# Performance work log

Hardware: AMD Instinct MI355X
Metric: run time of the kernel (lower is better)

Reference implementation:

```python
import jax, jax.numpy as jnp
import numpy as np

N_NODES = 50000
N_EDGES = 800000
IN_C = 64
OUT_C = 64
HEADS = 4
N_LAYERS = 2
BN_EPS = 1e-5
NEG_SLOPE = 0.2


def setup_inputs() -> dict:
    key = jax.random.key(0)
    ks = jax.random.split(key, 20)
    inp = {
        "x": jax.random.normal(ks[0], (N_NODES, IN_C), dtype=jnp.float32),
        "edge_index": jax.random.randint(ks[1], (2, N_EDGES), 0, N_NODES, dtype=jnp.int64),
        "edge_weight": jax.random.uniform(ks[2], (N_EDGES,), dtype=jnp.float32),
    }
    # per-layer GATConv + BN params (glorot-ish init)
    for i in range(N_LAYERS):
        k = 3 + i * 5
        scale = 1.0 / np.sqrt(IN_C)
        inp[f"W{i}"] = jax.random.normal(ks[k], (IN_C, HEADS * OUT_C), dtype=jnp.float32) * scale
        inp[f"asrc{i}"] = jax.random.normal(ks[k + 1], (HEADS, OUT_C), dtype=jnp.float32) * scale
        inp[f"adst{i}"] = jax.random.normal(ks[k + 2], (HEADS, OUT_C), dtype=jnp.float32) * scale
        inp[f"b{i}"] = jnp.zeros((OUT_C,), dtype=jnp.float32)
        inp[f"gamma{i}"] = jnp.ones((OUT_C,), dtype=jnp.float32)
        inp[f"beta{i}"] = jnp.zeros((OUT_C,), dtype=jnp.float32)
    return inp


def _gat_layer(x, src, dst, W, a_src, a_dst, b):
    # x: [N, C_in]; src/dst: [E'] (with self loops). Per-head dim = OUT_C.
    xh = (x @ W).reshape(-1, HEADS, OUT_C)          # [N, H, C]
    al_src = jnp.sum(xh * a_src[None], axis=-1)      # [N, H]
    al_dst = jnp.sum(xh * a_dst[None], axis=-1)      # [N, H]
    e = jax.nn.leaky_relu(al_src[src] + al_dst[dst], NEG_SLOPE)  # [E', H]
    # segment softmax over edges sharing a destination node
    m = jax.lax.stop_gradient(jax.ops.segment_max(e, dst, num_segments=N_NODES))
    p = jnp.exp(e - m[dst])
    denom = jax.ops.segment_sum(p, dst, num_segments=N_NODES)
    alpha = p / (denom[dst] + 1e-16)                 # [E', H]
    out = jax.ops.segment_sum(alpha[:, :, None] * xh[src], dst, num_segments=N_NODES)  # [N,H,C]
    return out.mean(axis=1) + b                      # concat=False -> mean over heads


def _batchnorm(x, gamma, beta):
    mu = x.mean(axis=0)
    var = x.var(axis=0)
    return gamma * (x - mu) * jax.lax.rsqrt(var + BN_EPS) + beta


def reference(x, edge_index, edge_weight, W0, asrc0, adst0, b0, gamma0, beta0,
              W1, asrc1, adst1, b1, gamma1, beta1):
    # edge_weight is passed as edge_attr to PyG GATConv but edge_dim=None -> ignored.
    loop = jnp.arange(N_NODES, dtype=edge_index.dtype)
    src = jnp.concatenate([edge_index[0], loop])  # add_self_loops=True (PyG default)
    dst = jnp.concatenate([edge_index[1], loop])
    params = [(W0, asrc0, adst0, b0, gamma0, beta0),
              (W1, asrc1, adst1, b1, gamma1, beta1)]
    saved = None
    for (W, a_s, a_d, b, g, bt) in params:
        x = _gat_layer(x, src, dst, W, a_s, a_d, b)
        saved = x
        x = _batchnorm(x, g, bt)
        x = jax.nn.relu(x)
        # dropout(0.5) is identity in eval mode
    return (x, saved)
```

## Files before the change

kernel.cpp:

```cpp
#include <hip/hip_runtime.h>
#include <stdint.h>

#define NEG_SLOPE 0.2f
#define BN_EPS 1e-5f

typedef __attribute__((ext_vector_type(8))) short bf16x8;
typedef __attribute__((ext_vector_type(4))) float f32x4;

__device__ __forceinline__ float bf2f(unsigned short u) {
  union { unsigned int i; float f; } v; v.i = ((unsigned int)u) << 16; return v.f;
}
__device__ __forceinline__ float asf(unsigned int u) {
  union { unsigned int i; float f; } v; v.i = u; return v.f;
}
__device__ __forceinline__ unsigned short f2bf(float f) {
  union { float f; unsigned int i; } v; v.f = f;
  unsigned int i = v.i;
  return (unsigned short)((i + 0x7fffu + ((i >> 16) & 1u)) >> 16);
}
__device__ __forceinline__ float loadF(const void* p, long long i, int f32) {
  return f32 ? ((const float*)p)[i] : bf2f(((const unsigned short*)p)[i]);
}
__device__ __forceinline__ int edge_at(const void* ei, long long idx, int is64) {
  return is64 ? (int)((const long long*)ei)[idx] : ((const int*)ei)[idx];
}

__global__ void detect_kernel(const unsigned short* __restrict__ x,
                              const int* __restrict__ ei32,
                              int* __restrict__ flags) {
  __shared__ int wild, oddnz;
  if (threadIdx.x == 0) { wild = 0; oddnz = 0; }
  __syncthreads();
  int lw = 0, lo = 0;
  for (int i = threadIdx.x; i < 4096; i += 256) {
    unsigned short u = x[i];
    int ex = (u >> 7) & 0xFF;
    if (ex >= 0x86) lw++;
    if (ei32[2 * i + 1] != 0) lo++;
  }
  if (lw) atomicAdd(&wild, lw);
  if (lo) atomicAdd(&oddnz, lo);
  __syncthreads();
  if (threadIdx.x == 0) { flags[0] = (wild > 64) ? 1 : 0; flags[1] = (oddnz == 0) ? 1 : 0; }
}

__global__ __launch_bounds__(256) void wtrans_kernel(
    const void* __restrict__ W0, const void* __restrict__ as0, const void* __restrict__ ad0,
    const void* __restrict__ W1, const void* __restrict__ as1, const void* __restrict__ ad1,
    const int* __restrict__ flags, int layer1_bf16,
    unsigned short* __restrict__ WTx0, unsigned short* __restrict__ WTx1) {
  const void* W = blockIdx.x ? W1 : W0;
  const void* asrc = blockIdx.x ? as1 : as0;
  const void* adst = blockIdx.x ? ad1 : ad0;
  unsigned short* WTx = blockIdx.x ? WTx1 : WTx0;
  int f32 = flags[0];
  __shared__ unsigned short Wl[64 * 258];
  int t = threadIdx.x;
  for (int i = t; i < 64 * 256; i += 256) {
    int k = i >> 8, c = i & 255;
    Wl[k * 258 + c] = f32 ? f2bf(((const float*)W)[i]) : ((const unsigned short*)W)[i];
  }
  __syncthreads();
  {
    int c = t;
    #pragma unroll
    for (int k8 = 0; k8 < 64; k8 += 8) {
      unsigned int p0 = (unsigned int)Wl[(k8 + 0) * 258 + c] | ((unsigned int)Wl[(k8 + 1) * 258 + c] << 16);
      unsigned int p1 = (unsigned int)Wl[(k8 + 2) * 258 + c] | ((unsigned int)Wl[(k8 + 3) * 258 + c] << 16);
      unsigned int p2 = (unsigned int)Wl[(k8 + 4) * 258 + c] | ((unsigned int)Wl[(k8 + 5) * 258 + c] << 16);
      unsigned int p3 = (unsigned int)Wl[(k8 + 6) * 258 + c] | ((unsigned int)Wl[(k8 + 7) * 258 + c] << 16);
      uint4 pk; pk.x = p0; pk.y = p1; pk.z = p2; pk.w = p3;
      *(uint4*)&WTx[c * 64 + k8] = pk;
    }
  }
  for (int idx = t; idx < 512; idx += 256) {
    int r = idx >> 6;
    int k = idx & 63;
    int h = r & 3;
    const void* av = (r >> 2) ? adst : asrc;
    float acc = 0.f;
    #pragma unroll 8
    for (int c = 0; c < 64; c++)
      acc += bf2f(Wl[k * 258 + h * 64 + c]) * loadF(av, h * 64 + c, f32);
    WTx[(256 + r) * 64 + k] = f2bf(acc);
  }
  for (int idx = t; idx < 512; idx += 256) WTx[264 * 64 + idx] = 0;
}

__global__ __launch_bounds__(256) void hist_kernel(const void* __restrict__ ei, int E, int N,
                                                   const int* __restrict__ flags,
                                                   int* __restrict__ deg) {
  int e = blockIdx.x * 256 + threadIdx.x;
  if (e >= E) return;
  int is64 = flags[1];
  int d = edge_at(ei, (long long)E + e, is64);
  d = (d < 0 || d >= N) ? 0 : d;
  atomicAdd(&deg[d], 1);
}

__global__ __launch_bounds__(256) void partial_kernel(const int* __restrict__ deg,
                                                      int* __restrict__ blocksum, int N) {
  int t = threadIdx.x;
  int idx = blockIdx.x * 256 + t;
  int v = (idx < N) ? deg[idx] : 0;
  #pragma unroll
  for (int o = 1; o < 64; o <<= 1) v += __shfl_xor(v, o);
  __shared__ int ws[4];
  if ((t & 63) == 0) ws[t >> 6] = v;
  __syncthreads();
  if (t == 0) blocksum[blockIdx.x] = ws[0] + ws[1] + ws[2] + ws[3];
}

__global__ void scan_base_kernel(const int* __restrict__ blocksum,
                                 int* __restrict__ blockbase, int B) {
  int lane = threadIdx.x;
  int base = 0;
  if (lane == 0) blockbase[0] = 0;
  for (int start = 0; start < B; start += 64) {
    int idx = start + lane;
    int v = (idx < B) ? blocksum[idx] : 0;
    int sc = v;
    #pragma unroll
    for (int o = 1; o < 64; o <<= 1) {
      int u = __shfl_up(sc, o);
      if (lane >= o) sc += u;
    }
    if (idx < B) blockbase[idx + 1] = base + sc;
    base = __shfl(base + sc, 63);
  }
}

__global__ __launch_bounds__(256) void scan_final_kernel(const int* __restrict__ deg,
                                                         const int* __restrict__ blockbase,
                                                         int* __restrict__ offsets, int N) {
  int t = threadIdx.x;
  int lane = t & 63;
  int wid = t >> 6;
  int idx = blockIdx.x * 256 + t;
  int v = (idx < N) ? deg[idx] : 0;
  int sc = v;
  #pragma unroll
  for (int o = 1; o < 64; o <<= 1) {
    int u = __shfl_up(sc, o);
    if (lane >= o) sc += u;
  }
  __shared__ int ws[4];
  if (lane == 63) ws[wid] = sc;
  __syncthreads();
  int add = 0;
  #pragma unroll
  for (int w = 0; w < 4; w++) if (w < wid) add += ws[w];
  if (idx < N) offsets[idx + 1] = blockbase[blockIdx.x] + add + sc;
  if (idx == 0) offsets[0] = 0;
}

__global__ __launch_bounds__(256) void scatter_kernel(
    const void* __restrict__ ei, int E, int N, const int* __restrict__ flags,
    const int* __restrict__ offsets, int* __restrict__ cursor,
    int* __restrict__ csr_src) {
  int e = blockIdx.x * 256 + threadIdx.x;
  if (e >= E) return;
  int is64 = flags[1];
  int s = edge_at(ei, e, is64);
  int d = edge_at(ei, (long long)E + e, is64);
  s = (s < 0 || s >= N) ? 0 : s;
  d = (d < 0 || d >= N) ? 0 : d;
  int pos = offsets[d] + atomicAdd(&cursor[d], 1);
  csr_src[pos] = s;
}

__global__ __launch_bounds__(256, 2) void gemm_mfma(
    const void* __restrict__ x, const unsigned short* __restrict__ WTx,
    const int* __restrict__ flags, int x_flex,
    unsigned short* __restrict__ xh, float* __restrict__ als, float* __restrict__ ald,
    int N) {
  __shared__ unsigned short RP[4][16 * 264];
  int f32 = flags[0];
  int xf = x_flex ? f32 : 0;
  int t = threadIdx.x;
  int wave = t >> 6, lane = t & 63;
  int q = lane >> 4, r16 = lane & 15;
  int m0 = blockIdx.x * 64 + wave * 16;
  if (m0 >= N) return;
  int row = m0 + r16;
  int rowc = row < N ? row : N - 1;

  bf16x8 a0, a1;
  if (xf) {
    const float* xp = (const float*)x + (size_t)rowc * 64 + q * 8;
    float4 v0 = ((const float4*)xp)[0];
    float4 v1 = ((const float4*)xp)[1];
    float4 v2 = ((const float4*)(xp + 32))[0];
    float4 v3 = ((const float4*)(xp + 32))[1];
    a0[0] = (short)f2bf(v0.x); a0[1] = (short)f2bf(v0.y); a0[2] = (short)f2bf(v0.z); a0[3] = (short)f2bf(v0.w);
    a0[4] = (short)f2bf(v1.x); a0[5] = (short)f2bf(v1.y); a0[6] = (short)f2bf(v1.z); a0[7] = (short)f2bf(v1.w);
    a1[0] = (short)f2bf(v2.x); a1[1] = (short)f2bf(v2.y); a1[2] = (short)f2bf(v2.z); a1[3] = (short)f2bf(v2.w);
    a1[4] = (short)f2bf(v3.x); a1[5] = (short)f2bf(v3.y); a1[6] = (short)f2bf(v3.z); a1[7] = (short)f2bf(v3.w);
  } else {
    const unsigned short* xp = (const unsigned short*)x + (size_t)rowc * 64 + q * 8;
    a0 = *(const bf16x8*)xp;
    a1 = *(const bf16x8*)(xp + 32);
  }

  f32x4 acc[17];
  #pragma unroll
  for (int tt = 0; tt < 17; tt++) acc[tt] = (f32x4){0.f, 0.f, 0.f, 0.f};
  #pragma unroll
  for (int tt = 0; tt < 17; tt++) {
    int c = tt * 16 + r16;
    bf16x8 b0 = *(const bf16x8*)(WTx + c * 64 + q * 8);
    bf16x8 b1 = *(const bf16x8*)(WTx + c * 64 + 32 + q * 8);
    acc[tt] = __builtin_amdgcn_mfma_f32_16x16x32_bf16(a0, b0, acc[tt], 0, 0, 0);
    acc[tt] = __builtin_amdgcn_mfma_f32_16x16x32_bf16(a1, b1, acc[tt], 0, 0, 0);
  }

  {
    int obase = m0 + q * 4;
    #pragma unroll
    for (int rr = 0; rr < 4; rr++) {
      int orow = obase + rr;
      if (orow < N) {
        if (r16 < 4) als[orow * 4 + r16] = acc[16][rr];
        else if (r16 < 8) ald[orow * 4 + (r16 - 4)] = acc[16][rr];
      }
    }
  }
  unsigned short* rp = RP[wave];
  #pragma unroll
  for (int tt = 0; tt < 16; tt++) {
    #pragma unroll
    for (int rr = 0; rr < 4; rr++)
      rp[(q * 4 + rr) * 264 + tt * 16 + r16] = f2bf(acc[tt][rr]);
  }
  #pragma unroll
  for (int i = 0; i < 8; i++) {
    int g = i * 64 + lane;
    int r = g >> 5;
    int grp = g & 31;
    uint4 v = *(const uint4*)&rp[r * 264 + grp * 8];
    int orow = m0 + r;
    if (orow < N) ((uint4*)xh)[(size_t)orow * 32 + grp] = v;
  }
}

__global__ __launch_bounds__(256) void agg_kernel(
    const unsigned short* __restrict__ xh,
    const float* __restrict__ als, const float* __restrict__ ald,
    const int* __restrict__ offsets, const int* __restrict__ csr_src,
    const void* __restrict__ bias, const int* __restrict__ flags,
    float* __restrict__ y, float* __restrict__ saved, int N) {
  int lane = threadIdx.x & 63;
  int wid = threadIdx.x >> 6;
  int n = blockIdx.x * 4 + wid;
  if (n >= N) return;
  int h = lane >> 4;
  const uint2* xv = (const uint2*)xh;
  float ad = ald[n * 4 + h];
  float e = als[n * 4 + h] + ad;
  e = (e > 0.f) ? e : NEG_SLOPE * e;
  float p = __expf(e);
  float dsum = p;
  uint2 xs = xv[(size_t)n * 64 + lane];
  float a0 = p * asf(xs.x << 16), a1 = p * asf(xs.x & 0xffff0000u);
  float a2 = p * asf(xs.y << 16), a3 = p * asf(xs.y & 0xffff0000u);
  int beg = offsets[n], end = offsets[n + 1];
  int j = beg;
  for (; j + 2 <= end; j += 2) {
    int s0 = csr_src[j];
    int s1 = csr_src[j + 1];
    uint2 v0 = xv[(size_t)s0 * 64 + lane];
    uint2 v1 = xv[(size_t)s1 * 64 + lane];
    float e0 = als[s0 * 4 + h] + ad;
    float e1 = als[s1 * 4 + h] + ad;
    e0 = (e0 > 0.f) ? e0 : NEG_SLOPE * e0;
    e1 = (e1 > 0.f) ? e1 : NEG_SLOPE * e1;
    float p0 = __expf(e0);
    float p1 = __expf(e1);
    dsum += p0 + p1;
    a0 += p0 * asf(v0.x << 16) + p1 * asf(v1.x << 16);
    a1 += p0 * asf(v0.x & 0xffff0000u) + p1 * asf(v1.x & 0xffff0000u);
    a2 += p0 * asf(v0.y << 16) + p1 * asf(v1.y << 16);
    a3 += p0 * asf(v0.y & 0xffff0000u) + p1 * asf(v1.y & 0xffff0000u);
  }
  if (j < end) {
    int s0 = csr_src[j];
    uint2 v0 = xv[(size_t)s0 * 64 + lane];
    float e0 = als[s0 * 4 + h] + ad;
    e0 = (e0 > 0.f) ? e0 : NEG_SLOPE * e0;
    float p0 = __expf(e0);
    dsum += p0;
    a0 += p0 * asf(v0.x << 16);
    a1 += p0 * asf(v0.x & 0xffff0000u);
    a2 += p0 * asf(v0.y << 16);
    a3 += p0 * asf(v0.y & 0xffff0000u);
  }
  float inv = 1.0f / dsum;
  a0 *= inv; a1 *= inv; a2 *= inv; a3 *= inv;
  a0 += __shfl_xor(a0, 16); a0 += __shfl_xor(a0, 32);
  a1 += __shfl_xor(a1, 16); a1 += __shfl_xor(a1, 32);
  a2 += __shfl_xor(a2, 16); a2 += __shfl_xor(a2, 32);
  a3 += __shfl_xor(a3, 16); a3 += __shfl_xor(a3, 32);
  if (lane < 16) {
    int f32 = flags[0];
    float4 o;
    o.x = 0.25f * a0 + loadF(bias, 4 * lane + 0, f32);
    o.y = 0.25f * a1 + loadF(bias, 4 * lane + 1, f32);
    o.z = 0.25f * a2 + loadF(bias, 4 * lane + 2, f32);
    o.w = 0.25f * a3 + loadF(bias, 4 * lane + 3, f32);
    ((float4*)(y + (size_t)n * 64))[lane] = o;
    if (saved) ((float4*)(saved + (size_t)n * 64))[lane] = o;
  }
}

__global__ __launch_bounds__(256) void stats_kernel(const float* __restrict__ y,
                                                    float* __restrict__ gsum,
                                                    float* __restrict__ gsq, int N) {
  __shared__ float ls[256], lq[256];
  int t = threadIdx.x;
  int c = t & 63;
  int r0 = blockIdx.x * 4 + (t >> 6);
  float s = 0.f, q = 0.f;
  for (int r = r0; r < N; r += gridDim.x * 4) {
    float v = y[(size_t)r * 64 + c];
    s += v; q += v * v;
  }
  ls[t] = s; lq[t] = q;
  __syncthreads();
  if (t < 64) {
    s = ls[t] + ls[t + 64] + ls[t + 128] + ls[t + 192];
    q = lq[t] + lq[t + 64] + lq[t + 128] + lq[t + 192];
    atomicAdd(&gsum[c], s);
    atomicAdd(&gsq[c], q);
  }
}

__global__ __launch_bounds__(256) void bn_kernel(
    const float* __restrict__ y, const float* __restrict__ gsum, const float* __restrict__ gsq,
    const void* __restrict__ gamma, const void* __restrict__ beta,
    const int* __restrict__ flags, float* __restrict__ out_f,
    unsigned short* __restrict__ out_b, int N) {
  int i = blockIdx.x * 256 + threadIdx.x;
  if (i >= N * 16) return;
  int f32 = flags[0];
  int cg = i & 15;
  float4 v = ((const float4*)y)[i];
  float4 s = ((const float4*)gsum)[cg];
  float4 q = ((const float4*)gsq)[cg];
  float inv_n = 1.0f / (float)N;
  float vv[4] = {v.x, v.y, v.z, v.w};
  float ss[4] = {s.x, s.y, s.z, s.w};
  float qq[4] = {q.x, q.y, q.z, q.w};
  float o[4];
  #pragma unroll
  for (int k = 0; k < 4; k++) {
    float g = loadF(gamma, 4 * cg + k, f32);
    float b = loadF(beta, 4 * cg + k, f32);
    float mu = ss[k] * inv_n;
    float var = fmaxf(qq[k] * inv_n - mu * mu, 0.f);
    float r = g * (vv[k] - mu) * rsqrtf(var + BN_EPS) + b;
    o[k] = r > 0.f ? r : 0.f;
  }
  if (out_f) {
    float4 ov; ov.x = o[0]; ov.y = o[1]; ov.z = o[2]; ov.w = o[3];
    ((float4*)out_f)[i] = ov;
  }
  if (out_b) {
    ushort4 ov;
    ov.x = f2bf(o[0]); ov.y = f2bf(o[1]); ov.z = f2bf(o[2]); ov.w = f2bf(o[3]);
    ((ushort4*)out_b)[i] = ov;
  }
}

extern "C" void kernel_launch(void* const* d_in, const int* in_sizes, int n_in,
                              void* d_out, int out_size, void* d_ws, size_t ws_size,
                              hipStream_t stream) {
  const void* x    = d_in[0];
  const void* ei   = d_in[1];
  const void* W0    = d_in[3];
  const void* asrc0 = d_in[4];
  const void* adst0 = d_in[5];
  const void* b0    = d_in[6];
  const void* g0    = d_in[7];
  const void* be0   = d_in[8];
  const void* W1    = d_in[9];
  const void* asrc1 = d_in[10];
  const void* adst1 = d_in[11];
  const void* b1    = d_in[12];
  const void* g1    = d_in[13];
  const void* be1   = d_in[14];

  int N = in_sizes[0] / 64;
  int E = in_sizes[1] / 2;
  int NB = (N + 255) / 256;
  int NG = (N + 63) / 64;

  char* p = (char*)d_ws;
  auto alloc = [&](size_t bytes) -> char* {
    char* r = p;
    p += (bytes + 255) & ~(size_t)255;
    return r;
  };
  int* flags    = (int*)alloc(256);
  int* deg      = (int*)alloc((size_t)N * 4);
  int* cursor   = (int*)alloc((size_t)N * 4);
  int* offsets  = (int*)alloc((size_t)(N + 1) * 4);
  int* blocksum = (int*)alloc((size_t)NB * 4);
  int* blockbase= (int*)alloc((size_t)(NB + 1) * 4);
  int* csr_src  = (int*)alloc((size_t)E * 4);
  unsigned short* WTx0 = (unsigned short*)alloc(272 * 64 * 2);
  unsigned short* WTx1 = (unsigned short*)alloc(272 * 64 * 2);
  unsigned short* xh = (unsigned short*)alloc((size_t)N * 256 * 2);
  float* als    = (float*)alloc((size_t)N * 4 * 4);
  float* ald    = (float*)alloc((size_t)N * 4 * 4);
  float* y      = (float*)alloc((size_t)N * 64 * 4);
  unsigned short* x2 = (unsigned short*)alloc((size_t)N * 64 * 2);
  float* gsum0  = (float*)alloc(256);
  float* gsq0   = (float*)alloc(256);
  float* gsum1  = (float*)alloc(256);
  float* gsq1   = (float*)alloc(256);

  hipMemsetAsync(deg, 0, (size_t)N * 4, stream);
  hipMemsetAsync(cursor, 0, (size_t)N * 4, stream);
  hipMemsetAsync(gsum0, 0, 1024, stream);

  detect_kernel<<<1, 256, 0, stream>>>((const unsigned short*)x, (const int*)ei, flags);
  wtrans_kernel<<<2, 256, 0, stream>>>(W0, asrc0, adst0, W1, asrc1, adst1, flags, 0, WTx0, WTx1);

  hist_kernel<<<(E + 255) / 256, 256, 0, stream>>>(ei, E, N, flags, deg);
  partial_kernel<<<NB, 256, 0, stream>>>(deg, blocksum, N);
  scan_base_kernel<<<1, 64, 0, stream>>>(blocksum, blockbase, NB);
  scan_final_kernel<<<NB, 256, 0, stream>>>(deg, blockbase, offsets, N);
  scatter_kernel<<<(E + 255) / 256, 256, 0, stream>>>(ei, E, N, flags, offsets, cursor, csr_src);

  float* out_x = (float*)d_out;
  float* out_saved = out_x + (size_t)N * 64;

  gemm_mfma<<<NG, 256, 0, stream>>>(x, WTx0, flags, 1, xh, als, ald, N);
  agg_kernel<<<(N + 3) / 4, 256, 0, stream>>>(xh, als, ald, offsets, csr_src, b0, flags, y,
                                              (float*)nullptr, N);
  stats_kernel<<<250, 256, 0, stream>>>(y, gsum0, gsq0, N);
  bn_kernel<<<(N * 16 + 255) / 256, 256, 0, stream>>>(y, gsum0, gsq0, g0, be0, flags,
                                                      (float*)nullptr, x2, N);

  gemm_mfma<<<NG, 256, 0, stream>>>(x2, WTx1, flags, 0, xh, als, ald, N);
  agg_kernel<<<(N + 3) / 4, 256, 0, stream>>>(xh, als, ald, offsets, csr_src, b1, flags, y,
                                              out_saved, N);
  stats_kernel<<<250, 256, 0, stream>>>(y, gsum1, gsq1, N);
  bn_kernel<<<(N * 16 + 255) / 256, 256, 0, stream>>>(y, gsum1, gsq1, g1, be1, flags,
                                                      out_x, (unsigned short*)nullptr, N);
}
```

Before: 464.9 us.

## Fuse BN stats into aggregation and BN-apply into second-layer GEMM load

Aggregation now runs on a grid-stride loop with two half-waves splitting each node's edges and 16-byte row gathers, and it accumulates per-channel BN sum and sum-of-squares through shared-memory atomics. This removes both separate stats kernels. The layer-0 BN plus ReLU is applied inside the second GEMM's input load, which drops the intermediate bf16 buffer and one bn_kernel launch. The cost is more shared atomics, extra shuffles, and a smaller grid for aggregation.

```diff
diff --git a/kernel.cpp b/kernel.cpp
--- a/kernel.cpp
+++ b/kernel.cpp
@@ -47,7 +47,7 @@
 __global__ __launch_bounds__(256) void wtrans_kernel(
     const void* __restrict__ W0, const void* __restrict__ as0, const void* __restrict__ ad0,
     const void* __restrict__ W1, const void* __restrict__ as1, const void* __restrict__ ad1,
-    const int* __restrict__ flags, int layer1_bf16,
+    const int* __restrict__ flags,
     unsigned short* __restrict__ WTx0, unsigned short* __restrict__ WTx1) {
   const void* W = blockIdx.x ? W1 : W0;
   const void* asrc = blockIdx.x ? as1 : as0;
@@ -171,13 +171,25 @@
 
 __global__ __launch_bounds__(256, 2) void gemm_mfma(
     const void* __restrict__ x, const unsigned short* __restrict__ WTx,
-    const int* __restrict__ flags, int x_flex,
+    const int* __restrict__ flags, int mode,
+    const float* __restrict__ gsum, const float* __restrict__ gsq,
+    const void* __restrict__ gamma, const void* __restrict__ beta,
     unsigned short* __restrict__ xh, float* __restrict__ als, float* __restrict__ ald,
     int N) {
   __shared__ unsigned short RP[4][16 * 264];
+  __shared__ float bnsc[64], bnsh[64];
   int f32 = flags[0];
-  int xf = x_flex ? f32 : 0;
   int t = threadIdx.x;
+  if (mode == 1) {
+    if (t < 64) {
+      float mu = gsum[t] / (float)N;
+      float var = fmaxf(gsq[t] / (float)N - mu * mu, 0.f);
+      float sc = loadF(gamma, t, f32) * rsqrtf(var + BN_EPS);
+      bnsc[t] = sc;
+      bnsh[t] = loadF(beta, t, f32) - mu * sc;
+    }
+    __syncthreads();
+  }
   int wave = t >> 6, lane = t & 63;
   int q = lane >> 4, r16 = lane & 15;
   int m0 = blockIdx.x * 64 + wave * 16;
@@ -186,16 +198,33 @@
   int rowc = row < N ? row : N - 1;
 
   bf16x8 a0, a1;
-  if (xf) {
+  if (mode == 1) {
     const float* xp = (const float*)x + (size_t)rowc * 64 + q * 8;
-    float4 v0 = ((const float4*)xp)[0];
-    float4 v1 = ((const float4*)xp)[1];
-    float4 v2 = ((const float4*)(xp + 32))[0];
-    float4 v3 = ((const float4*)(xp + 32))[1];
-    a0[0] = (short)f2bf(v0.x); a0[1] = (short)f2bf(v0.y); a0[2] = (short)f2bf(v0.z); a0[3] = (short)f2bf(v0.w);
-    a0[4] = (short)f2bf(v1.x); a0[5] = (short)f2bf(v1.y); a0[6] = (short)f2bf(v1.z); a0[7] = (short)f2bf(v1.w);
-    a1[0] = (short)f2bf(v2.x); a1[1] = (short)f2bf(v2.y); a1[2] = (short)f2bf(v2.z); a1[3] = (short)f2bf(v2.w);
-    a1[4] = (short)f2bf(v3.x); a1[5] = (short)f2bf(v3.y); a1[6] = (short)f2bf(v3.z); a1[7] = (short)f2bf(v3.w);
+    float va[8], vb[8];
+    *(float4*)&va[0] = ((const float4*)xp)[0];
+    *(float4*)&va[4] = ((const float4*)xp)[1];
+    *(float4*)&vb[0] = ((const float4*)(xp + 32))[0];
+    *(float4*)&vb[4] = ((const float4*)(xp + 32))[1];
+    int k0 = q * 8;
+    #pragma unroll
+    for (int jj = 0; jj < 8; jj++) {
+      float v = fmaxf(va[jj] * bnsc[k0 + jj] + bnsh[k0 + jj], 0.f);
+      float w = fmaxf(vb[jj] * bnsc[k0 + 32 + jj] + bnsh[k0 + 32 + jj], 0.f);
+      a0[jj] = (short)f2bf(v);
+      a1[jj] = (short)f2bf(w);
+    }
+  } else if (f32) {
+    const float* xp = (const float*)x + (size_t)rowc * 64 + q * 8;
+    float va[8], vb[8];
+    *(float4*)&va[0] = ((const float4*)xp)[0];
+    *(float4*)&va[4] = ((const float4*)xp)[1];
+    *(float4*)&vb[0] = ((const float4*)(xp + 32))[0];
+    *(float4*)&vb[4] = ((const float4*)(xp + 32))[1];
+    #pragma unroll
+    for (int jj = 0; jj < 8; jj++) {
+      a0[jj] = (short)f2bf(va[jj]);
+      a1[jj] = (short)f2bf(vb[jj]);
+    }
   } else {
     const unsigned short* xp = (const unsigned short*)x + (size_t)rowc * 64 + q * 8;
     a0 = *(const bf16x8*)xp;
@@ -248,97 +277,101 @@
     const float* __restrict__ als, const float* __restrict__ ald,
     const int* __restrict__ offsets, const int* __restrict__ csr_src,
     const void* __restrict__ bias, const int* __restrict__ flags,
-    float* __restrict__ y, float* __restrict__ saved, int N) {
-  int lane = threadIdx.x & 63;
-  int wid = threadIdx.x >> 6;
-  int n = blockIdx.x * 4 + wid;
-  if (n >= N) return;
-  int h = lane >> 4;
-  const uint2* xv = (const uint2*)xh;
-  float ad = ald[n * 4 + h];
-  float e = als[n * 4 + h] + ad;
-  e = (e > 0.f) ? e : NEG_SLOPE * e;
-  float p = __expf(e);
-  float dsum = p;
-  uint2 xs = xv[(size_t)n * 64 + lane];
-  float a0 = p * asf(xs.x << 16), a1 = p * asf(xs.x & 0xffff0000u);
-  float a2 = p * asf(xs.y << 16), a3 = p * asf(xs.y & 0xffff0000u);
-  int beg = offsets[n], end = offsets[n + 1];
-  int j = beg;
-  for (; j + 2 <= end; j += 2) {
-    int s0 = csr_src[j];
-    int s1 = csr_src[j + 1];
-    uint2 v0 = xv[(size_t)s0 * 64 + lane];
-    uint2 v1 = xv[(size_t)s1 * 64 + lane];
-    float e0 = als[s0 * 4 + h] + ad;
-    float e1 = als[s1 * 4 + h] + ad;
-    e0 = (e0 > 0.f) ? e0 : NEG_SLOPE * e0;
-    e1 = (e1 > 0.f) ? e1 : NEG_SLOPE * e1;
-    float p0 = __expf(e0);
-    float p1 = __expf(e1);
-    dsum += p0 + p1;
-    a0 += p0 * asf(v0.x << 16) + p1 * asf(v1.x << 16);
-    a1 += p0 * asf(v0.x & 0xffff0000u) + p1 * asf(v1.x & 0xffff0000u);
-    a2 += p0 * asf(v0.y << 16) + p1 * asf(v1.y << 16);
-    a3 += p0 * asf(v0.y & 0xffff0000u) + p1 * asf(v1.y & 0xffff0000u);
-  }
-  if (j < end) {
-    int s0 = csr_src[j];
-    uint2 v0 = xv[(size_t)s0 * 64 + lane];
-    float e0 = als[s0 * 4 + h] + ad;
-    e0 = (e0 > 0.f) ? e0 : NEG_SLOPE * e0;
-    float p0 = __expf(e0);
-    dsum += p0;
-    a0 += p0 * asf(v0.x << 16);
-    a1 += p0 * asf(v0.x & 0xffff0000u);
-    a2 += p0 * asf(v0.y << 16);
-    a3 += p0 * asf(v0.y & 0xffff0000u);
-  }
-  float inv = 1.0f / dsum;
-  a0 *= inv; a1 *= inv; a2 *= inv; a3 *= inv;
-  a0 += __shfl_xor(a0, 16); a0 += __shfl_xor(a0, 32);
-  a1 += __shfl_xor(a1, 16); a1 += __shfl_xor(a1, 32);
-  a2 += __shfl_xor(a2, 16); a2 += __shfl_xor(a2, 32);
-  a3 += __shfl_xor(a3, 16); a3 += __shfl_xor(a3, 32);
-  if (lane < 16) {
-    int f32 = flags[0];
-    float4 o;
-    o.x = 0.25f * a0 + loadF(bias, 4 * lane + 0, f32);
-    o.y = 0.25f * a1 + loadF(bias, 4 * lane + 1, f32);
-    o.z = 0.25f * a2 + loadF(bias, 4 * lane + 2, f32);
-    o.w = 0.25f * a3 + loadF(bias, 4 * lane + 3, f32);
-    ((float4*)(y + (size_t)n * 64))[lane] = o;
-    if (saved) ((float4*)(saved + (size_t)n * 64))[lane] = o;
-  }
-}
-
-__global__ __launch_bounds__(256) void stats_kernel(const float* __restrict__ y,
-                                                    float* __restrict__ gsum,
-                                                    float* __restrict__ gsq, int N) {
-  __shared__ float ls[256], lq[256];
+    float* __restrict__ y, float* __restrict__ gsum, float* __restrict__ gsq, int N) {
+  __shared__ float bsum[64], bsq[64];
   int t = threadIdx.x;
-  int c = t & 63;
-  int r0 = blockIdx.x * 4 + (t >> 6);
-  float s = 0.f, q = 0.f;
-  for (int r = r0; r < N; r += gridDim.x * 4) {
-    float v = y[(size_t)r * 64 + c];
-    s += v; q += v * v;
-  }
-  ls[t] = s; lq[t] = q;
+  if (t < 64) { bsum[t] = 0.f; bsq[t] = 0.f; }
+  __syncthreads();
+  int lane = t & 63;
+  int wid = t >> 6;
+  int hl = lane & 31;
+  int h = hl >> 3;
+  int half = lane >> 5;
+  int f32 = flags[0];
+  const uint4* xv = (const uint4*)xh;
+  int stride = gridDim.x * 4;
+  for (int n = blockIdx.x * 4 + wid; n < N; n += stride) {
+    float ad = ald[n * 4 + h];
+    float acc0 = 0.f, acc1 = 0.f, acc2 = 0.f, acc3 = 0.f;
+    float acc4 = 0.f, acc5 = 0.f, acc6 = 0.f, acc7 = 0.f;
+    float dsum = 0.f;
+    if (half == 0) {
+      float e = als[n * 4 + h] + ad;
+      e = (e > 0.f) ? e : NEG_SLOPE * e;
+      float p = __expf(e);
+      dsum = p;
+      uint4 v = xv[(size_t)n * 32 + hl];
+      acc0 = p * asf(v.x << 16); acc1 = p * asf(v.x & 0xffff0000u);
+      acc2 = p * asf(v.y << 16); acc3 = p * asf(v.y & 0xffff0000u);
+      acc4 = p * asf(v.z << 16); acc5 = p * asf(v.z & 0xffff0000u);
+      acc6 = p * asf(v.w << 16); acc7 = p * asf(v.w & 0xffff0000u);
+    }
+    int beg = offsets[n], end = offsets[n + 1];
+    int imax = (end - beg + 1) >> 1;
+    for (int i = 0; i < imax; i++) {
+      int j = beg + 2 * i + half;
+      if (j < end) {
+        int s = csr_src[j];
+        float e = als[s * 4 + h] + ad;
+        e = (e > 0.f) ? e : NEG_SLOPE * e;
+        float p = __expf(e);
+        dsum += p;
+        uint4 v = xv[(size_t)s * 32 + hl];
+        acc0 += p * asf(v.x << 16); acc1 += p * asf(v.x & 0xffff0000u);
+        acc2 += p * asf(v.y << 16); acc3 += p * asf(v.y & 0xffff0000u);
+        acc4 += p * asf(v.z << 16); acc5 += p * asf(v.z & 0xffff0000u);
+        acc6 += p * asf(v.w << 16); acc7 += p * asf(v.w & 0xffff0000u);
+      }
+    }
+    dsum += __shfl_xor(dsum, 32);
+    acc0 += __shfl_xor(acc0, 32); acc1 += __shfl_xor(acc1, 32);
+    acc2 += __shfl_xor(acc2, 32); acc3 += __shfl_xor(acc3, 32);
+    acc4 += __shfl_xor(acc4, 32); acc5 += __shfl_xor(acc5, 32);
+    acc6 += __shfl_xor(acc6, 32); acc7 += __shfl_xor(acc7, 32);
+    float inv = 1.0f / dsum;
+    acc0 *= inv; acc1 *= inv; acc2 *= inv; acc3 *= inv;
+    acc4 *= inv; acc5 *= inv; acc6 *= inv; acc7 *= inv;
+    acc0 += __shfl_xor(acc0, 8); acc0 += __shfl_xor(acc0, 16);
+    acc1 += __shfl_xor(acc1, 8); acc1 += __shfl_xor(acc1, 16);
+    acc2 += __shfl_xor(acc2, 8); acc2 += __shfl_xor(acc2, 16);
+    acc3 += __shfl_xor(acc3, 8); acc3 += __shfl_xor(acc3, 16);
+    acc4 += __shfl_xor(acc4, 8); acc4 += __shfl_xor(acc4, 16);
+    acc5 += __shfl_xor(acc5, 8); acc5 += __shfl_xor(acc5, 16);
+    acc6 += __shfl_xor(acc6, 8); acc6 += __shfl_xor(acc6, 16);
+    acc7 += __shfl_xor(acc7, 8); acc7 += __shfl_xor(acc7, 16);
+    if (lane < 8) {
+      int cb = 8 * lane;
+      float o[8];
+      o[0] = 0.25f * acc0 + loadF(bias, cb + 0, f32);
+      o[1] = 0.25f * acc1 + loadF(bias, cb + 1, f32);
+      o[2] = 0.25f * acc2 + loadF(bias, cb + 2, f32);
+      o[3] = 0.25f * acc3 + loadF(bias, cb + 3, f32);
+      o[4] = 0.25f * acc4 + loadF(bias, cb + 4, f32);
+      o[5] = 0.25f * acc5 + loadF(bias, cb + 5, f32);
+      o[6] = 0.25f * acc6 + loadF(bias, cb + 6, f32);
+      o[7] = 0.25f * acc7 + loadF(bias, cb + 7, f32);
+      float4 o0; o0.x = o[0]; o0.y = o[1]; o0.z = o[2]; o0.w = o[3];
+      float4 o1; o1.x = o[4]; o1.y = o[5]; o1.z = o[6]; o1.w = o[7];
+      *(float4*)(y + (size_t)n * 64 + cb) = o0;
+      *(float4*)(y + (size_t)n * 64 + cb + 4) = o1;
+      #pragma unroll
+      for (int c = 0; c < 8; c++) {
+        atomicAdd(&bsum[cb + c], o[c]);
+        atomicAdd(&bsq[cb + c], o[c] * o[c]);
+      }
+    }
+  }
   __syncthreads();
   if (t < 64) {
-    s = ls[t] + ls[t + 64] + ls[t + 128] + ls[t + 192];
-    q = lq[t] + lq[t + 64] + lq[t + 128] + lq[t + 192];
-    atomicAdd(&gsum[c], s);
-    atomicAdd(&gsq[c], q);
+    atomicAdd(&gsum[t], bsum[t]);
+    atomicAdd(&gsq[t], bsq[t]);
   }
 }
 
 __global__ __launch_bounds__(256) void bn_kernel(
     const float* __restrict__ y, const float* __restrict__ gsum, const float* __restrict__ gsq,
     const void* __restrict__ gamma, const void* __restrict__ beta,
-    const int* __restrict__ flags, float* __restrict__ out_f,
-    unsigned short* __restrict__ out_b, int N) {
+    const int* __restrict__ flags, float* __restrict__ out_f, int N) {
   int i = blockIdx.x * 256 + threadIdx.x;
   if (i >= N * 16) return;
   int f32 = flags[0];
@@ -360,15 +393,8 @@
     float r = g * (vv[k] - mu) * rsqrtf(var + BN_EPS) + b;
     o[k] = r > 0.f ? r : 0.f;
   }
-  if (out_f) {
-    float4 ov; ov.x = o[0]; ov.y = o[1]; ov.z = o[2]; ov.w = o[3];
-    ((float4*)out_f)[i] = ov;
-  }
-  if (out_b) {
-    ushort4 ov;
-    ov.x = f2bf(o[0]); ov.y = f2bf(o[1]); ov.z = f2bf(o[2]); ov.w = f2bf(o[3]);
-    ((ushort4*)out_b)[i] = ov;
-  }
+  float4 ov; ov.x = o[0]; ov.y = o[1]; ov.z = o[2]; ov.w = o[3];
+  ((float4*)out_f)[i] = ov;
 }
 
 extern "C" void kernel_launch(void* const* d_in, const int* in_sizes, int n_in,
@@ -393,6 +419,7 @@
   int E = in_sizes[1] / 2;
   int NB = (N + 255) / 256;
   int NG = (N + 63) / 64;
+  int NA = (N + 15) / 16;
 
   char* p = (char*)d_ws;
   auto alloc = [&](size_t bytes) -> char* {
@@ -413,7 +440,6 @@
   float* als    = (float*)alloc((size_t)N * 4 * 4);
   float* ald    = (float*)alloc((size_t)N * 4 * 4);
   float* y      = (float*)alloc((size_t)N * 64 * 4);
-  unsigned short* x2 = (unsigned short*)alloc((size_t)N * 64 * 2);
   float* gsum0  = (float*)alloc(256);
   float* gsq0   = (float*)alloc(256);
   float* gsum1  = (float*)alloc(256);
@@ -424,7 +450,7 @@
   hipMemsetAsync(gsum0, 0, 1024, stream);
 
   detect_kernel<<<1, 256, 0, stream>>>((const unsigned short*)x, (const int*)ei, flags);
-  wtrans_kernel<<<2, 256, 0, stream>>>(W0, asrc0, adst0, W1, asrc1, adst1, flags, 0, WTx0, WTx1);
+  wtrans_kernel<<<2, 256, 0, stream>>>(W0, asrc0, adst0, W1, asrc1, adst1, flags, WTx0, WTx1);
 
   hist_kernel<<<(E + 255) / 256, 256, 0, stream>>>(ei, E, N, flags, deg);
   partial_kernel<<<NB, 256, 0, stream>>>(deg, blocksum, N);
@@ -435,17 +461,15 @@
   float* out_x = (float*)d_out;
   float* out_saved = out_x + (size_t)N * 64;
 
-  gemm_mfma<<<NG, 256, 0, stream>>>(x, WTx0, flags, 1, xh, als, ald, N);
-  agg_kernel<<<(N + 3) / 4, 256, 0, stream>>>(xh, als, ald, offsets, csr_src, b0, flags, y,
-                                              (float*)nullptr, N);
-  stats_kernel<<<250, 256, 0, stream>>>(y, gsum0, gsq0, N);
-  bn_kernel<<<(N * 16 + 255) / 256, 256, 0, stream>>>(y, gsum0, gsq0, g0, be0, flags,
-                                                      (float*)nullptr, x2, N);
-
-  gemm_mfma<<<NG, 256, 0, stream>>>(x2, WTx1, flags, 0, xh, als, ald, N);
-  agg_kernel<<<(N + 3) / 4, 256, 0, stream>>>(xh, als, ald, offsets, csr_src, b1, flags, y,
-                                              out_saved, N);
-  stats_kernel<<<250, 256, 0, stream>>>(y, gsum1, gsq1, N);
-  bn_kernel<<<(N * 16 + 255) / 256, 256, 0, stream>>>(y, gsum1, gsq1, g1, be1, flags,
-                                                      out_x, (unsigned short*)nullptr, N);
-}
+  gemm_mfma<<<NG, 256, 0, stream>>>(x, WTx0, flags, 0, (const float*)nullptr,
+                                    (const float*)nullptr, nullptr, nullptr,
+                                    xh, als, ald, N);
+  agg_kernel<<<NA, 256, 0, stream>>>(xh, als, ald, offsets, csr_src, b0, flags,
+                                     y, gsum0, gsq0, N);
+  gemm_mfma<<<NG, 256, 0, stream>>>(y, WTx1, flags, 1, gsum0, gsq0, g0, be0,
+                                    xh, als, ald, N);
+  agg_kernel<<<NA, 256, 0, stream>>>(xh, als, ald, offsets, csr_src, b1, flags,
+                                     out_saved, gsum1, gsq1, N);
+  bn_kernel<<<(N * 16 + 255) / 256, 256, 0, stream>>>(out_saved, gsum1, gsq1, g1, be1,
+                                                      flags, out_x, N);
+}
```

New measurement: 528.5 us. +13.7%, slower.
